# Kernel optimization log

Measured on AMD Instinct MI355X. Metric: run time of the kernel, lower is better.

The kernel has to match this reference:

```python
import jax, jax.numpy as jnp
import numpy as np

NUM_HEADS = 4
FEAT_DIM = 128
EMBED_DIM = 128
B, K, C, H, W = 2, 8, 128, 128, 128


def _cross_attn(Qf, Kf, Vf, qw, qb, kw, kb, aqw, aqb, akw, akb):
    """Faithful port of PixelCrossAttentionRefiner._cross_attn.
    Qf: [B, Cq, H, W]; Kf: [B, K, Ck, H, W]; Vf: [B, K, C, H, W].
    Uses only the (head-averaged) softmax weights of MultiheadAttention,
    L2-renormalizes them, then takes a weighted sum of RAW values.
    """
    b, _, h, w = Qf.shape
    k_cand = Kf.shape[1]
    bn = b * h * w
    # Query: per-pixel feature vector -> q1 projection -> attn in-proj (query part)
    Query = jnp.transpose(Qf, (0, 2, 3, 1)).reshape(bn, -1)            # [BN, Cq]
    q = Query @ qw.T + qb                                               # [BN, E]
    # Key: NOTE torch does .permute(0,1,3,4,2).reshape(B*N, K, -1) which is a
    # flat row-major reinterpretation of the (B,K,H,W,Ck) buffer; jnp reshape
    # after transpose has identical semantics, so this is bit-faithful.
    Key = jnp.transpose(Kf, (0, 1, 3, 4, 2)).reshape(bn, k_cand, -1)    # [BN, K, Ck]
    kk = Key @ kw.T + kb                                                # [BN, K, E]
    # nn.MultiheadAttention internal in-projections (value path is dead code)
    qa = q @ aqw.T + aqb                                                # [BN, E]
    ka = kk @ akw.T + akb                                               # [BN, K, E]
    e = qa.shape[-1]
    dh = e // NUM_HEADS
    qh = qa.reshape(bn, NUM_HEADS, dh)
    kh = ka.reshape(bn, k_cand, NUM_HEADS, dh)
    scale = 1.0 / np.sqrt(dh).astype(np.float32)
    scores = jnp.einsum('mhd,mkhd->mhk', qh, kh) * scale                # [BN, H, K]
    attw = jax.nn.softmax(scores, axis=-1).mean(axis=1)                 # avg heads -> [BN, K]
    # F.normalize(p=2, dim=-1, eps=1e-12)
    attw = attw / jnp.maximum(jnp.linalg.norm(attw, axis=-1, keepdims=True), 1e-12)
    Value = jnp.transpose(Vf, (0, 1, 3, 4, 2)).reshape(bn, k_cand, -1)  # [BN, K, C]
    out = jnp.einsum('mk,mkc->mc', attw, Value)                         # [BN, C]
    return jnp.transpose(out.reshape(b, h, w, -1), (0, 3, 1, 2))        # [B, C, H, W]


def _forward(HF_star, HF_cands, Z_cands,
             q1_w, q1_b, k1_w, k1_b, a1_qw, a1_qb, a1_kw, a1_kb,
             q2_w, q2_b, k2_w, k2_b, a2_qw, a2_qb, a2_kw, a2_kb):
    b, c, h, w = HF_star.shape
    k_cand = HF_cands.shape[1]
    i = jnp.linspace(0.0, 1.0, h, dtype=HF_star.dtype)
    j = jnp.linspace(0.0, 1.0, w, dtype=HF_star.dtype)
    ig, jg = jnp.meshgrid(i, j, indexing='ij')
    ig = jnp.broadcast_to(ig[None, None], (b, 1, h, w))
    jg = jnp.broadcast_to(jg[None, None], (b, 1, h, w))
    Q1 = jnp.concatenate([HF_star, ig, jg], axis=1)                     # [B, C+2, H, W]
    ik = jnp.broadcast_to(ig[:, None], (b, k_cand, 1, h, w))
    jk = jnp.broadcast_to(jg[:, None], (b, k_cand, 1, h, w))
    K1 = jnp.concatenate([HF_cands, ik, jk], axis=2)                    # [B, K, C+2, H, W]
    z_star = _cross_attn(Q1, K1, Z_cands, q1_w, q1_b, k1_w, k1_b,
                         a1_qw, a1_qb, a1_kw, a1_kb)                    # [B, C, H, W]
    z_exp = jnp.broadcast_to(z_star[:, None], (b, k_cand, c, h, w))
    Q2 = jnp.concatenate([HF_star, z_star, ig, jg], axis=1)             # [B, 2C+2, H, W]
    K2 = jnp.concatenate([HF_cands, z_exp, ik, jk], axis=2)             # [B, K, 2C+2, H, W]
    z_hat = _cross_attn(Q2, K2, Z_cands, q2_w, q2_b, k2_w, k2_b,
                        a2_qw, a2_qb, a2_kw, a2_kb)
    return z_star, z_hat


def setup_inputs() -> dict:
    key = jax.random.key(0)
    ks = jax.random.split(key, 16)
    E = EMBED_DIM
    d1 = FEAT_DIM + 2
    d2 = 2 * FEAT_DIM + 2

    def lin(k, fan_out, fan_in):
        bound = 1.0 / np.sqrt(fan_in)
        kw, kb = jax.random.split(k)
        return (jax.random.uniform(kw, (fan_out, fan_in), jnp.float32, -bound, bound),
                jax.random.uniform(kb, (fan_out,), jnp.float32, -bound, bound))

    q1_w, q1_b = lin(ks[0], E, d1)
    k1_w, k1_b = lin(ks[1], E, d1)
    q2_w, q2_b = lin(ks[2], E, d2)
    k2_w, k2_b = lin(ks[3], E, d2)
    a1_qw, a1_qb = lin(ks[4], E, E)
    a1_kw, a1_kb = lin(ks[5], E, E)
    a2_qw, a2_qb = lin(ks[6], E, E)
    a2_kw, a2_kb = lin(ks[7], E, E)
    return {
        'HF_star': jax.random.normal(ks[8], (B, C, H, W), jnp.float32),
        'HF_cands': jax.random.normal(ks[9], (B, K, C, H, W), jnp.float32),
        'Z_cands': jax.random.normal(ks[10], (B, K, C, H, W), jnp.float32),
        'q1_w': q1_w, 'q1_b': q1_b, 'k1_w': k1_w, 'k1_b': k1_b,
        'a1_qw': a1_qw, 'a1_qb': a1_qb, 'a1_kw': a1_kw, 'a1_kb': a1_kb,
        'q2_w': q2_w, 'q2_b': q2_b, 'k2_w': k2_w, 'k2_b': k2_b,
        'a2_qw': a2_qw, 'a2_qb': a2_qb, 'a2_kw': a2_kw, 'a2_kb': a2_kb,
    }


def reference(HF_star, HF_cands, Z_cands,
              q1_w, q1_b, k1_w, k1_b, a1_qw, a1_qb, a1_kw, a1_kb,
              q2_w, q2_b, k2_w, k2_b, a2_qw, a2_qb, a2_kw, a2_kb):
    return _forward(HF_star, HF_cands, Z_cands,
                    q1_w, q1_b, k1_w, k1_b, a1_qw, a1_qb, a1_kw, a1_kb,
                    q2_w, q2_b, k2_w, k2_b, a2_qw, a2_qb, a2_kw, a2_kb)
```

## Files before the change

### kernel.cpp

```cpp
#include <hip/hip_runtime.h>
#include <math.h>

constexpr int Bc = 2, Kc = 8, HWc = 16384;
constexpr float SCALE  = 0.17677669529663687f;
constexpr float INV127 = 1.0f / 127.0f;

using short8 = __attribute__((ext_vector_type(8))) short;
using f32x4  = __attribute__((ext_vector_type(4))) float;

constexpr int OWQ1 = 0;
constexpr int OBQ1 = OWQ1 + 130 * 128;
constexpr int OWK1 = OBQ1 + 128;
constexpr int OBK1 = OWK1 + 130 * 128;
constexpr int OWQ2 = OBK1 + 128;
constexpr int OBQ2 = OWQ2 + 258 * 128;
constexpr int OWK2 = OBQ2 + 128;
constexpr int OBK2 = OWK2 + 258 * 128;
constexpr int OPACK = OBK2 + 128;
constexpr int PQ1 = 0;
constexpr int PQ2 = PQ1 + 32 * 512;
constexpr int PY1 = PQ2 + 64 * 512;
constexpr int PY2 = PY1 + 32 * 512;

__device__ __forceinline__ unsigned bfpack(float a, float b) {
    unsigned ua = __float_as_uint(a); ua = (ua + 0x7FFFu + ((ua >> 16) & 1u)) >> 16;
    unsigned ub = __float_as_uint(b); ub = (ub + 0x7FFFu + ((ub >> 16) & 1u)) >> 16;
    return ua | (ub << 16);
}
__device__ __forceinline__ short bf1(float a) {
    unsigned ua = __float_as_uint(a); ua = (ua + 0x7FFFu + ((ua >> 16) & 1u)) >> 16;
    return (short)ua;
}
__device__ __forceinline__ float bflo(unsigned u) { return __uint_as_float(u << 16); }
__device__ __forceinline__ float bfhi(unsigned u) { return __uint_as_float(u & 0xFFFF0000u); }
__device__ __forceinline__ float bf2f(short s) {
    return __uint_as_float(((unsigned)(unsigned short)s) << 16);
}

__global__ __launch_bounds__(128) void prep_kernel(
    const float* __restrict__ q1w, const float* __restrict__ q1b,
    const float* __restrict__ k1w, const float* __restrict__ k1b,
    const float* __restrict__ a1qw, const float* __restrict__ a1qb,
    const float* __restrict__ a1kw, const float* __restrict__ a1kb,
    const float* __restrict__ q2w, const float* __restrict__ q2b,
    const float* __restrict__ k2w, const float* __restrict__ k2b,
    const float* __restrict__ a2qw, const float* __restrict__ a2qb,
    const float* __restrict__ a2kw, const float* __restrict__ a2kb,
    float* __restrict__ ws)
{
    const int job = blockIdx.x / 260;
    const int d   = blockIdx.x % 260;
    const float *aw, *ab, *w, *wb;
    float *owt, *ob;
    int D;
    if (job == 0)      { aw=a1qw; ab=a1qb; w=q1w; wb=q1b; owt=ws+OWQ1; ob=ws+OBQ1; D=130; }
    else if (job == 1) { aw=a1kw; ab=a1kb; w=k1w; wb=k1b; owt=ws+OWK1; ob=ws+OBK1; D=130; }
    else if (job == 2) { aw=a2qw; ab=a2qb; w=q2w; wb=q2b; owt=ws+OWQ2; ob=ws+OBQ2; D=258; }
    else               { aw=a2kw; ab=a2kb; w=k2w; wb=k2b; owt=ws+OWK2; ob=ws+OBK2; D=258; }
    const int e = threadIdx.x;
    if (d < D) {
        float acc = 0.f;
        for (int f = 0; f < 128; ++f) acc += aw[e * 128 + f] * w[f * D + d];
        owt[d * 128 + e] = acc;
    } else if (d == D) {
        float acc = ab[e];
        for (int f = 0; f < 128; ++f) acc += aw[e * 128 + f] * wb[f];
        ob[e] = acc;
    }
}

__global__ __launch_bounds__(64) void pack_kernel(float* __restrict__ ws)
{
    short* pk = (short*)(ws + OPACK);
    const int l = threadIdx.x, bid = blockIdx.x;
    const float* w;
    short* dst;
    short v[8];
    if (bid < 32) {
        const int et = bid >> 2, kt = bid & 3;
        w = ws + OWQ1;
        dst = pk + PQ1 + ((size_t)(et * 4 + kt) * 64 + l) * 8;
        #pragma unroll
        for (int idx = 0; idx < 8; ++idx)
            v[idx] = bf1(w[(kt * 32 + (l >> 4) * 8 + idx) * 128 + et * 16 + (l & 15)]);
    } else if (bid < 96) {
        const int b2 = bid - 32, et = b2 >> 3, kt = b2 & 7;
        w = ws + OWQ2;
        dst = pk + PQ2 + ((size_t)(et * 8 + kt) * 64 + l) * 8;
        #pragma unroll
        for (int idx = 0; idx < 8; ++idx)
            v[idx] = bf1(w[(kt * 32 + (l >> 4) * 8 + idx) * 128 + et * 16 + (l & 15)]);
    } else if (bid < 128) {
        const int b2 = bid - 96, ct = b2 >> 2, h = b2 & 3;
        w = ws + OWK1;
        dst = pk + PY1 + ((size_t)(ct * 4 + h) * 64 + l) * 8;
        #pragma unroll
        for (int idx = 0; idx < 8; ++idx)
            v[idx] = bf1(w[(ct * 16 + (l & 15)) * 128 + h * 32 + (l >> 4) * 8 + idx]);
    } else {
        const int b2 = bid - 128, ct = b2 >> 2, h = b2 & 3;
        w = ws + OWK2;
        dst = pk + PY2 + ((size_t)(ct * 4 + h) * 64 + l) * 8;
        #pragma unroll
        for (int idx = 0; idx < 8; ++idx)
            v[idx] = bf1(w[(ct * 16 + (l & 15)) * 128 + h * 32 + (l >> 4) * 8 + idx]);
    }
    uint4 u;
    u.x = (unsigned)(unsigned short)v[0] | ((unsigned)(unsigned short)v[1] << 16);
    u.y = (unsigned)(unsigned short)v[2] | ((unsigned)(unsigned short)v[3] << 16);
    u.z = (unsigned)(unsigned short)v[4] | ((unsigned)(unsigned short)v[5] << 16);
    u.w = (unsigned)(unsigned short)v[6] | ((unsigned)(unsigned short)v[7] << 16);
    *(uint4*)dst = u;
}

template <int STAGE>
__global__ __launch_bounds__(256) void stage_kernel(
    const float* __restrict__ HFs,
    const float* __restrict__ HFc,
    const float* __restrict__ Zc,
    const float* __restrict__ ws,
    const float* __restrict__ zst,
    float* __restrict__ out)
{
    constexpr int CQ  = (STAGE == 1) ? 128 : 256;
    constexpr int CK  = CQ;
    constexpr int NP  = CK / 128;
    constexpr int NKT = CQ / 32;

    const float* qwt = ws + ((STAGE == 1) ? OWQ1 : OWQ2);
    const float* qb_ = ws + ((STAGE == 1) ? OBQ1 : OBQ2);
    const float* kwt = ws + ((STAGE == 1) ? OWK1 : OWK2);
    const float* kb_ = ws + ((STAGE == 1) ? OBK1 : OBK2);
    const short* pk  = (const short*)(ws + OPACK);
    const short* aQ  = pk + ((STAGE == 1) ? PQ1 : PQ2);
    const short* aY  = pk + ((STAGE == 1) ? PY1 : PY2);

    __shared__ __align__(16) char smem[27136];
    short* sXF = (short*)smem;
    uint2* sYQ = (uint2*)smem;
    float* sRed = (float*)smem;
    short* sQF = (short*)(smem + 17408);
    float* sYX = (float*)(smem + 21504);
    float* sHW = sYX + 192;
    float* sSc = sHW + 576;
    float* sAW = sSc + 512;

    const int t   = threadIdx.x;
    const int l   = t & 63;
    const int wv  = t >> 6;
    const int bid = blockIdx.x;
    const int b   = bid >> 10;
    const int rem = bid & 1023;
    const int ks  = rem >> 7;
    const int hp  = rem & 127;
    const int r0  = ks * 2048 + hp * 16;

    const float ik = (float)hp * INV127;
    const float iq = (float)(r0 >> 7) * INV127;
    const int   w0 = r0 & 127;

    {
        const int qg = t & 3, c = t >> 2;
        #pragma unroll
        for (int r = 0; r < CQ / 64; ++r) {
            const int cc = c + r * 64;
            const float* src = (STAGE == 1 || cc < 128)
                ? HFs + ((size_t)(b * 128 + cc)) * HWc + r0 + qg * 4
                : zst + ((size_t)(b * 128 + (cc - 128))) * HWc + r0 + qg * 4;
            const float4 x = *(const float4*)src;
            const int kt = cc >> 5, g = (cc & 31) >> 3, idx = cc & 7;
            short* dstb = &sXF[kt * 512 + idx + 16 * g * 8];
            dstb[(qg * 4 + 0) * 8] = bf1(x.x);
            dstb[(qg * 4 + 1) * 8] = bf1(x.y);
            dstb[(qg * 4 + 2) * 8] = bf1(x.z);
            dstb[(qg * 4 + 3) * 8] = bf1(x.w);
        }
    }
    __syncthreads();

    {
        const float jqv = (float)(w0 + (l & 15)) * INV127;
        f32x4 acc0, acc1;
        #pragma unroll
        for (int r = 0; r < 4; ++r) {
            const int e0 = (wv * 2 + 0) * 16 + (l >> 4) * 4 + r;
            const int e1 = (wv * 2 + 1) * 16 + (l >> 4) * 4 + r;
            acc0[r] = qb_[e0] + iq * qwt[(size_t)CQ * 128 + e0]
                             + jqv * qwt[(size_t)(CQ + 1) * 128 + e0];
            acc1[r] = qb_[e1] + iq * qwt[(size_t)CQ * 128 + e1]
                             + jqv * qwt[(size_t)(CQ + 1) * 128 + e1];
        }
        #pragma unroll
        for (int kt = 0; kt < NKT; ++kt) {
            const short8 bfr = *(const short8*)&sXF[kt * 512 + l * 8];
            const short8 a0 = *(const short8*)&aQ[(((wv * 2 + 0) * NKT + kt) * 64 + l) * 8];
            const short8 a1 = *(const short8*)&aQ[(((wv * 2 + 1) * NKT + kt) * 64 + l) * 8];
            acc0 = __builtin_amdgcn_mfma_f32_16x16x32_bf16(a0, bfr, acc0, 0, 0, 0);
            acc1 = __builtin_amdgcn_mfma_f32_16x16x32_bf16(a1, bfr, acc1, 0, 0, 0);
        }
        #pragma unroll
        for (int m = 0; m < 2; ++m) {
            const f32x4 a = m ? acc1 : acc0;
            const int e0 = (wv * 2 + m) * 16 + (l >> 4) * 4;
            const int kt = e0 >> 5, g = (e0 & 31) >> 3, idx0 = e0 & 7;
            uint2 u; u.x = bfpack(a[0], a[1]); u.y = bfpack(a[2], a[3]);
            *(uint2*)&sQF[kt * 512 + ((l & 15) + 16 * g) * 8 + idx0] = u;
        }
    }
    __syncthreads();

    if (t < 192) {
        const int q = t & 15, h = (t >> 4) & 3, which = t >> 6;
        const float* wrow = (which == 0) ? kwt + (size_t)CK * 128
                          : (which == 1) ? kwt + (size_t)(CK + 1) * 128
                                         : kb_;
        float acc = 0.f;
        #pragma unroll
        for (int e32 = 0; e32 < 32; ++e32) {
            const int e2 = h * 32 + e32;
            const int g = (e2 & 31) >> 3, idx = e2 & 7;
            acc += wrow[e2] * bf2f(sQF[h * 512 + (q + 16 * g) * 8 + idx]);
        }
        sYX[(which * 4 + h) * 16 + q] = acc;
    }

    short8 bq0 = *(const short8*)&sQF[0 * 512 + l * 8];
    short8 bq1 = *(const short8*)&sQF[1 * 512 + l * 8];
    short8 bq2 = *(const short8*)&sQF[2 * 512 + l * 8];
    short8 bq3 = *(const short8*)&sQF[3 * 512 + l * 8];

    const int pg = t & 31;
    const int cs = t >> 5;
    const int q  = pg >> 1;
    float acc[4][4];
    #pragma unroll
    for (int h = 0; h < 4; ++h)
        #pragma unroll
        for (int j = 0; j < 4; ++j) acc[h][j] = 0.f;
    const f32x4 zf = {0.f, 0.f, 0.f, 0.f};

    #pragma unroll
    for (int p = 0; p < NP; ++p) {
        #pragma unroll
        for (int m = 0; m < 2; ++m) {
            const int ctl = wv * 2 + m;
            const int ct  = p * 8 + ctl;
            f32x4 d0, d1, d2, d3;
            {
                const short8 a0 = *(const short8*)&aY[(((ct * 4) + 0) * 64 + l) * 8];
                const short8 a1 = *(const short8*)&aY[(((ct * 4) + 1) * 64 + l) * 8];
                const short8 a2 = *(const short8*)&aY[(((ct * 4) + 2) * 64 + l) * 8];
                const short8 a3 = *(const short8*)&aY[(((ct * 4) + 3) * 64 + l) * 8];
                d0 = __builtin_amdgcn_mfma_f32_16x16x32_bf16(a0, bq0, zf, 0, 0, 0);
                d1 = __builtin_amdgcn_mfma_f32_16x16x32_bf16(a1, bq1, zf, 0, 0, 0);
                d2 = __builtin_amdgcn_mfma_f32_16x16x32_bf16(a2, bq2, zf, 0, 0, 0);
                d3 = __builtin_amdgcn_mfma_f32_16x16x32_bf16(a3, bq3, zf, 0, 0, 0);
            }
            #pragma unroll
            for (int r = 0; r < 4; ++r) {
                const int cl = ctl * 16 + (l >> 4) * 4 + r;
                uint2 u;
                u.x = bfpack(d0[r], d1[r]);
                u.y = bfpack(d2[r], d3[r]);
                sYQ[cl * 17 + (l & 15)] = u;
            }
        }
        __syncthreads();

        {
            const int cbase = p * 128 + cs * 16;
            const float* xp = (STAGE == 1 || cbase < 128)
                ? HFc + (((size_t)(b * Kc + ks)) * 128 + cbase) * HWc + hp * 128 + pg * 4
                : zst + ((size_t)(b * 128 + (cbase - 128))) * HWc + hp * 128 + pg * 4;
            const uint2* yqp = &sYQ[(cs * 16) * 17 + q];
            #pragma unroll 8
            for (int cc = 0; cc < 16; ++cc) {
                const float4 x = *(const float4*)(xp + (size_t)cc * HWc);
                const uint2 u = yqp[cc * 17];
                const float y0 = bflo(u.x), y1 = bfhi(u.x);
                const float y2 = bflo(u.y), y3 = bfhi(u.y);
                acc[0][0] += y0 * x.x; acc[0][1] += y0 * x.y;
                acc[0][2] += y0 * x.z; acc[0][3] += y0 * x.w;
                acc[1][0] += y1 * x.x; acc[1][1] += y1 * x.y;
                acc[1][2] += y1 * x.z; acc[1][3] += y1 * x.w;
                acc[2][0] += y2 * x.x; acc[2][1] += y2 * x.y;
                acc[2][2] += y2 * x.z; acc[2][3] += y2 * x.w;
                acc[3][0] += y3 * x.x; acc[3][1] += y3 * x.y;
                acc[3][2] += y3 * x.z; acc[3][3] += y3 * x.w;
            }
        }
        __syncthreads();
    }

    #pragma unroll
    for (int h = 0; h < 4; ++h)
        #pragma unroll
        for (int j = 0; j < 4; ++j)
            acc[h][j] += __shfl_xor(acc[h][j], 32, 64);
    if (l < 32) {
        #pragma unroll
        for (int h = 0; h < 4; ++h)
            #pragma unroll
            for (int j = 0; j < 4; ++j)
                sRed[wv * 512 + pg * 16 + h * 4 + j] = acc[h][j];
    }
    __syncthreads();

    if (t < 128) {
        const int pos = t, pgg = pos >> 2, j = pos & 3, qq = pos >> 3;
        const float jk = (float)pos * INV127;
        #pragma unroll
        for (int h = 0; h < 4; ++h) {
            const float v = sRed[0 * 512 + pgg * 16 + h * 4 + j]
                          + sRed[1 * 512 + pgg * 16 + h * 4 + j]
                          + sRed[2 * 512 + pgg * 16 + h * 4 + j]
                          + sRed[3 * 512 + pgg * 16 + h * 4 + j];
            const float s = v + ik * sYX[(0 * 4 + h) * 16 + qq]
                              + jk * sYX[(1 * 4 + h) * 16 + qq]
                              +      sYX[(2 * 4 + h) * 16 + qq];
            sSc[h * 128 + pos] = s * SCALE;
        }
    }
    __syncthreads();

    if (t < 64) {
        const int qq = t & 15, h = t >> 4;
        float sc[8], m = -INFINITY;
        #pragma unroll
        for (int j = 0; j < 8; ++j) {
            sc[j] = sSc[h * 128 + qq * 8 + j];
            m = fmaxf(m, sc[j]);
        }
        float sum = 0.f;
        #pragma unroll
        for (int j = 0; j < 8; ++j) { sc[j] = __expf(sc[j] - m); sum += sc[j]; }
        const float inv = 0.25f / sum;
        #pragma unroll
        for (int j = 0; j < 8; ++j) sHW[(h * 16 + qq) * 9 + j] = sc[j] * inv;
    }
    __syncthreads();
    if (t < 16) {
        float at[8];
        float n2 = 0.f;
        #pragma unroll
        for (int j = 0; j < 8; ++j) {
            at[j] = sHW[(0 * 16 + t) * 9 + j] + sHW[(1 * 16 + t) * 9 + j]
                  + sHW[(2 * 16 + t) * 9 + j] + sHW[(3 * 16 + t) * 9 + j];
            n2 += at[j] * at[j];
        }
        const float nrm = fmaxf(sqrtf(n2), 1e-12f);
        #pragma unroll
        for (int j = 0; j < 8; ++j) sAW[t * 8 + j] = at[j] / nrm;
    }
    __syncthreads();

    {
        const int idx = t & 15, cg = t >> 4;
        const int c8  = cg * 8;
        const float4 a0 = *(const float4*)&sAW[idx * 8];
        const float4 a1 = *(const float4*)&sAW[idx * 8 + 4];
        const float* zb = Zc + (((size_t)(b * Kc + ks)) * 128 + c8) * HWc + hp * 128 + idx * 8;
        float* ob = out + ((size_t)(b * 128 + c8)) * HWc + r0 + idx;
        #pragma unroll
        for (int i = 0; i < 8; ++i) {
            const float4 z0 = *(const float4*)(zb + (size_t)i * HWc);
            const float4 z1 = *(const float4*)(zb + (size_t)i * HWc + 4);
            ob[(size_t)i * HWc] =
                a0.x * z0.x + a0.y * z0.y + a0.z * z0.z + a0.w * z0.w +
                a1.x * z1.x + a1.y * z1.y + a1.z * z1.z + a1.w * z1.w;
        }
    }
}

extern "C" void kernel_launch(void* const* d_in, const int* in_sizes, int n_in,
                              void* d_out, int out_size, void* d_ws, size_t ws_size,
                              hipStream_t stream)
{
    const float* HFs = (const float*)d_in[0];
    const float* HFc = (const float*)d_in[1];
    const float* Zc  = (const float*)d_in[2];
    float* ws    = (float*)d_ws;
    float* zstar = (float*)d_out;
    float* zhat  = zstar + (size_t)Bc * 128 * HWc;

    prep_kernel<<<1040, 128, 0, stream>>>(
        (const float*)d_in[3],  (const float*)d_in[4],
        (const float*)d_in[5],  (const float*)d_in[6],
        (const float*)d_in[7],  (const float*)d_in[8],
        (const float*)d_in[9],  (const float*)d_in[10],
        (const float*)d_in[11], (const float*)d_in[12],
        (const float*)d_in[13], (const float*)d_in[14],
        (const float*)d_in[15], (const float*)d_in[16],
        (const float*)d_in[17], (const float*)d_in[18],
        ws);

    pack_kernel<<<192, 64, 0, stream>>>(ws);

    stage_kernel<1><<<2048, 256, 0, stream>>>(HFs, HFc, Zc, ws, zstar, zstar);
    stage_kernel<2><<<2048, 256, 0, stream>>>(HFs, HFc, Zc, ws, zstar, zhat);
}
```

Measured before the change: 154.7 us.

## Process two candidate slices per block to reuse weight fragments and zstar loads

Each block now handles two adjacent candidate indices (ks0, ks0+1), which halves the grid to 1024 blocks. The query-projection and key-projection MFMA fragments are loaded once and applied to both slices. In stage 2 the zstar channel half of the key input is loaded once and shared by both accumulators. The cost is roughly double the register and shared-memory footprint per block (46 KB of LDS), which may lower occupancy and leave fewer blocks to fill the GPU.

```diff
diff --git a/kernel.cpp b/kernel.cpp
--- a/kernel.cpp
+++ b/kernel.cpp
@@ -35,6 +35,14 @@
 __device__ __forceinline__ float bfhi(unsigned u) { return __uint_as_float(u & 0xFFFF0000u); }
 __device__ __forceinline__ float bf2f(short s) {
     return __uint_as_float(((unsigned)(unsigned short)s) << 16);
+}
+
+__device__ __forceinline__ void fma16(float (&a)[4][4], uint2 u, float4 x) {
+    const float y0 = bflo(u.x), y1 = bfhi(u.x), y2 = bflo(u.y), y3 = bfhi(u.y);
+    a[0][0] += y0 * x.x; a[0][1] += y0 * x.y; a[0][2] += y0 * x.z; a[0][3] += y0 * x.w;
+    a[1][0] += y1 * x.x; a[1][1] += y1 * x.y; a[1][2] += y1 * x.z; a[1][3] += y1 * x.w;
+    a[2][0] += y2 * x.x; a[2][1] += y2 * x.y; a[2][2] += y2 * x.z; a[2][3] += y2 * x.w;
+    a[3][0] += y3 * x.x; a[3][1] += y3 * x.y; a[3][2] += y3 * x.z; a[3][3] += y3 * x.w;
 }
 
 __global__ __launch_bounds__(128) void prep_kernel(
@@ -135,108 +143,135 @@
     const short* aQ  = pk + ((STAGE == 1) ? PQ1 : PQ2);
     const short* aY  = pk + ((STAGE == 1) ? PY1 : PY2);
 
-    __shared__ __align__(16) char smem[27136];
-    short* sXF = (short*)smem;
-    uint2* sYQ = (uint2*)smem;
+    __shared__ __align__(16) char smem[46080];
+    short* sXF0 = (short*)smem;
+    short* sXF1 = sXF0 + CQ * 16;
+    short* sQF0 = sXF0 + 2 * CQ * 16;
+    short* sQF1 = sQF0 + 2048;
+    uint2* sYQ0 = (uint2*)smem;
+    uint2* sYQ1 = sYQ0 + 128 * 17;
     float* sRed = (float*)smem;
-    short* sQF = (short*)(smem + 17408);
-    float* sYX = (float*)(smem + 21504);
-    float* sHW = sYX + 192;
-    float* sSc = sHW + 576;
-    float* sAW = sSc + 512;
+    float* sYX  = (float*)(smem + 34816);
+    float* sHW  = sYX + 384;
+    float* sSc  = sHW + 1152;
+    float* sAW  = sSc + 1024;
 
     const int t   = threadIdx.x;
     const int l   = t & 63;
     const int wv  = t >> 6;
     const int bid = blockIdx.x;
-    const int b   = bid >> 10;
-    const int rem = bid & 1023;
-    const int ks  = rem >> 7;
+    const int b   = bid >> 9;
+    const int rem = bid & 511;
+    const int kp  = rem >> 7;
     const int hp  = rem & 127;
-    const int r0  = ks * 2048 + hp * 16;
-
-    const float ik = (float)hp * INV127;
-    const float iq = (float)(r0 >> 7) * INV127;
-    const int   w0 = r0 & 127;
+    const int ks0 = kp * 2;
+    const int r00 = ks0 * 2048 + hp * 16;
+    const int r01 = r00 + 2048;
+
+    const float ik  = (float)hp * INV127;
+    const float iq0 = (float)(r00 >> 7) * INV127;
+    const float iq1 = (float)(r01 >> 7) * INV127;
+    const int   w0  = (hp & 7) * 16;
 
     {
         const int qg = t & 3, c = t >> 2;
         #pragma unroll
         for (int r = 0; r < CQ / 64; ++r) {
             const int cc = c + r * 64;
-            const float* src = (STAGE == 1 || cc < 128)
-                ? HFs + ((size_t)(b * 128 + cc)) * HWc + r0 + qg * 4
-                : zst + ((size_t)(b * 128 + (cc - 128))) * HWc + r0 + qg * 4;
-            const float4 x = *(const float4*)src;
             const int kt = cc >> 5, g = (cc & 31) >> 3, idx = cc & 7;
-            short* dstb = &sXF[kt * 512 + idx + 16 * g * 8];
-            dstb[(qg * 4 + 0) * 8] = bf1(x.x);
-            dstb[(qg * 4 + 1) * 8] = bf1(x.y);
-            dstb[(qg * 4 + 2) * 8] = bf1(x.z);
-            dstb[(qg * 4 + 3) * 8] = bf1(x.w);
+            #pragma unroll
+            for (int kk = 0; kk < 2; ++kk) {
+                const int r0 = kk ? r01 : r00;
+                const float* src = (STAGE == 1 || cc < 128)
+                    ? HFs + ((size_t)(b * 128 + cc)) * HWc + r0 + qg * 4
+                    : zst + ((size_t)(b * 128 + cc - 128)) * HWc + r0 + qg * 4;
+                const float4 x = *(const float4*)src;
+                short* dstb = (kk ? sXF1 : sXF0) + kt * 512 + idx + 16 * g * 8;
+                dstb[(qg * 4 + 0) * 8] = bf1(x.x);
+                dstb[(qg * 4 + 1) * 8] = bf1(x.y);
+                dstb[(qg * 4 + 2) * 8] = bf1(x.z);
+                dstb[(qg * 4 + 3) * 8] = bf1(x.w);
+            }
         }
     }
     __syncthreads();
 
     {
         const float jqv = (float)(w0 + (l & 15)) * INV127;
-        f32x4 acc0, acc1;
+        f32x4 a00, a01, a10, a11;
         #pragma unroll
         for (int r = 0; r < 4; ++r) {
             const int e0 = (wv * 2 + 0) * 16 + (l >> 4) * 4 + r;
             const int e1 = (wv * 2 + 1) * 16 + (l >> 4) * 4 + r;
-            acc0[r] = qb_[e0] + iq * qwt[(size_t)CQ * 128 + e0]
-                             + jqv * qwt[(size_t)(CQ + 1) * 128 + e0];
-            acc1[r] = qb_[e1] + iq * qwt[(size_t)CQ * 128 + e1]
-                             + jqv * qwt[(size_t)(CQ + 1) * 128 + e1];
+            const float wi0 = qwt[(size_t)CQ * 128 + e0];
+            const float wj0 = qwt[(size_t)(CQ + 1) * 128 + e0];
+            const float wi1 = qwt[(size_t)CQ * 128 + e1];
+            const float wj1 = qwt[(size_t)(CQ + 1) * 128 + e1];
+            a00[r] = qb_[e0] + iq0 * wi0 + jqv * wj0;
+            a01[r] = qb_[e1] + iq0 * wi1 + jqv * wj1;
+            a10[r] = qb_[e0] + iq1 * wi0 + jqv * wj0;
+            a11[r] = qb_[e1] + iq1 * wi1 + jqv * wj1;
         }
         #pragma unroll
         for (int kt = 0; kt < NKT; ++kt) {
-            const short8 bfr = *(const short8*)&sXF[kt * 512 + l * 8];
-            const short8 a0 = *(const short8*)&aQ[(((wv * 2 + 0) * NKT + kt) * 64 + l) * 8];
-            const short8 a1 = *(const short8*)&aQ[(((wv * 2 + 1) * NKT + kt) * 64 + l) * 8];
-            acc0 = __builtin_amdgcn_mfma_f32_16x16x32_bf16(a0, bfr, acc0, 0, 0, 0);
-            acc1 = __builtin_amdgcn_mfma_f32_16x16x32_bf16(a1, bfr, acc1, 0, 0, 0);
+            const short8 b0 = *(const short8*)&sXF0[kt * 512 + l * 8];
+            const short8 b1 = *(const short8*)&sXF1[kt * 512 + l * 8];
+            const short8 f0 = *(const short8*)&aQ[(((wv * 2 + 0) * NKT + kt) * 64 + l) * 8];
+            const short8 f1 = *(const short8*)&aQ[(((wv * 2 + 1) * NKT + kt) * 64 + l) * 8];
+            a00 = __builtin_amdgcn_mfma_f32_16x16x32_bf16(f0, b0, a00, 0, 0, 0);
+            a01 = __builtin_amdgcn_mfma_f32_16x16x32_bf16(f1, b0, a01, 0, 0, 0);
+            a10 = __builtin_amdgcn_mfma_f32_16x16x32_bf16(f0, b1, a10, 0, 0, 0);
+            a11 = __builtin_amdgcn_mfma_f32_16x16x32_bf16(f1, b1, a11, 0, 0, 0);
         }
         #pragma unroll
         for (int m = 0; m < 2; ++m) {
-            const f32x4 a = m ? acc1 : acc0;
             const int e0 = (wv * 2 + m) * 16 + (l >> 4) * 4;
             const int kt = e0 >> 5, g = (e0 & 31) >> 3, idx0 = e0 & 7;
-            uint2 u; u.x = bfpack(a[0], a[1]); u.y = bfpack(a[2], a[3]);
-            *(uint2*)&sQF[kt * 512 + ((l & 15) + 16 * g) * 8 + idx0] = u;
+            const f32x4 va = m ? a01 : a00;
+            const f32x4 vb = m ? a11 : a10;
+            uint2 u0; u0.x = bfpack(va[0], va[1]); u0.y = bfpack(va[2], va[3]);
+            uint2 u1; u1.x = bfpack(vb[0], vb[1]); u1.y = bfpack(vb[2], vb[3]);
+            *(uint2*)&sQF0[kt * 512 + ((l & 15) + 16 * g) * 8 + idx0] = u0;
+            *(uint2*)&sQF1[kt * 512 + ((l & 15) + 16 * g) * 8 + idx0] = u1;
         }
     }
     __syncthreads();
 
     if (t < 192) {
-        const int q = t & 15, h = (t >> 4) & 3, which = t >> 6;
+        const int qq = t & 15, h = (t >> 4) & 3, which = t >> 6;
         const float* wrow = (which == 0) ? kwt + (size_t)CK * 128
                           : (which == 1) ? kwt + (size_t)(CK + 1) * 128
                                          : kb_;
-        float acc = 0.f;
+        float acc0 = 0.f, acc1 = 0.f;
         #pragma unroll
         for (int e32 = 0; e32 < 32; ++e32) {
             const int e2 = h * 32 + e32;
             const int g = (e2 & 31) >> 3, idx = e2 & 7;
-            acc += wrow[e2] * bf2f(sQF[h * 512 + (q + 16 * g) * 8 + idx]);
-        }
-        sYX[(which * 4 + h) * 16 + q] = acc;
-    }
-
-    short8 bq0 = *(const short8*)&sQF[0 * 512 + l * 8];
-    short8 bq1 = *(const short8*)&sQF[1 * 512 + l * 8];
-    short8 bq2 = *(const short8*)&sQF[2 * 512 + l * 8];
-    short8 bq3 = *(const short8*)&sQF[3 * 512 + l * 8];
+            const float wr = wrow[e2];
+            acc0 += wr * bf2f(sQF0[h * 512 + (qq + 16 * g) * 8 + idx]);
+            acc1 += wr * bf2f(sQF1[h * 512 + (qq + 16 * g) * 8 + idx]);
+        }
+        sYX[0 * 192 + (which * 4 + h) * 16 + qq] = acc0;
+        sYX[1 * 192 + (which * 4 + h) * 16 + qq] = acc1;
+    }
+    const short8 bqa0 = *(const short8*)&sQF0[0 * 512 + l * 8];
+    const short8 bqa1 = *(const short8*)&sQF0[1 * 512 + l * 8];
+    const short8 bqa2 = *(const short8*)&sQF0[2 * 512 + l * 8];
+    const short8 bqa3 = *(const short8*)&sQF0[3 * 512 + l * 8];
+    const short8 bqb0 = *(const short8*)&sQF1[0 * 512 + l * 8];
+    const short8 bqb1 = *(const short8*)&sQF1[1 * 512 + l * 8];
+    const short8 bqb2 = *(const short8*)&sQF1[2 * 512 + l * 8];
+    const short8 bqb3 = *(const short8*)&sQF1[3 * 512 + l * 8];
+    __syncthreads();
 
     const int pg = t & 31;
     const int cs = t >> 5;
     const int q  = pg >> 1;
-    float acc[4][4];
+    float acc0[4][4], acc1[4][4];
     #pragma unroll
     for (int h = 0; h < 4; ++h)
         #pragma unroll
-        for (int j = 0; j < 4; ++j) acc[h][j] = 0.f;
+        for (int j = 0; j < 4; ++j) { acc0[h][j] = 0.f; acc1[h][j] = 0.f; }
     const f32x4 zf = {0.f, 0.f, 0.f, 0.f};
 
     #pragma unroll
@@ -245,48 +280,52 @@
         for (int m = 0; m < 2; ++m) {
             const int ctl = wv * 2 + m;
             const int ct  = p * 8 + ctl;
-            f32x4 d0, d1, d2, d3;
-            {
-                const short8 a0 = *(const short8*)&aY[(((ct * 4) + 0) * 64 + l) * 8];
-                const short8 a1 = *(const short8*)&aY[(((ct * 4) + 1) * 64 + l) * 8];
-                const short8 a2 = *(const short8*)&aY[(((ct * 4) + 2) * 64 + l) * 8];
-                const short8 a3 = *(const short8*)&aY[(((ct * 4) + 3) * 64 + l) * 8];
-                d0 = __builtin_amdgcn_mfma_f32_16x16x32_bf16(a0, bq0, zf, 0, 0, 0);
-                d1 = __builtin_amdgcn_mfma_f32_16x16x32_bf16(a1, bq1, zf, 0, 0, 0);
-                d2 = __builtin_amdgcn_mfma_f32_16x16x32_bf16(a2, bq2, zf, 0, 0, 0);
-                d3 = __builtin_amdgcn_mfma_f32_16x16x32_bf16(a3, bq3, zf, 0, 0, 0);
-            }
+            const short8 y0 = *(const short8*)&aY[(((ct * 4) + 0) * 64 + l) * 8];
+            const short8 y1 = *(const short8*)&aY[(((ct * 4) + 1) * 64 + l) * 8];
+            const short8 y2 = *(const short8*)&aY[(((ct * 4) + 2) * 64 + l) * 8];
+            const short8 y3 = *(const short8*)&aY[(((ct * 4) + 3) * 64 + l) * 8];
+            f32x4 d0 = __builtin_amdgcn_mfma_f32_16x16x32_bf16(y0, bqa0, zf, 0, 0, 0);
+            f32x4 d1 = __builtin_amdgcn_mfma_f32_16x16x32_bf16(y1, bqa1, zf, 0, 0, 0);
+            f32x4 d2 = __builtin_amdgcn_mfma_f32_16x16x32_bf16(y2, bqa2, zf, 0, 0, 0);
+            f32x4 d3 = __builtin_amdgcn_mfma_f32_16x16x32_bf16(y3, bqa3, zf, 0, 0, 0);
+            f32x4 e0 = __builtin_amdgcn_mfma_f32_16x16x32_bf16(y0, bqb0, zf, 0, 0, 0);
+            f32x4 e1 = __builtin_amdgcn_mfma_f32_16x16x32_bf16(y1, bqb1, zf, 0, 0, 0);
+            f32x4 e2 = __builtin_amdgcn_mfma_f32_16x16x32_bf16(y2, bqb2, zf, 0, 0, 0);
+            f32x4 e3 = __builtin_amdgcn_mfma_f32_16x16x32_bf16(y3, bqb3, zf, 0, 0, 0);
             #pragma unroll
             for (int r = 0; r < 4; ++r) {
                 const int cl = ctl * 16 + (l >> 4) * 4 + r;
-                uint2 u;
-                u.x = bfpack(d0[r], d1[r]);
-                u.y = bfpack(d2[r], d3[r]);
-                sYQ[cl * 17 + (l & 15)] = u;
+                uint2 u0; u0.x = bfpack(d0[r], d1[r]); u0.y = bfpack(d2[r], d3[r]);
+                uint2 u1; u1.x = bfpack(e0[r], e1[r]); u1.y = bfpack(e2[r], e3[r]);
+                sYQ0[cl * 17 + (l & 15)] = u0;
+                sYQ1[cl * 17 + (l & 15)] = u1;
             }
         }
         __syncthreads();
 
         {
-            const int cbase = p * 128 + cs * 16;
-            const float* xp = (STAGE == 1 || cbase < 128)
-                ? HFc + (((size_t)(b * Kc + ks)) * 128 + cbase) * HWc + hp * 128 + pg * 4
-                : zst + ((size_t)(b * 128 + (cbase - 128))) * HWc + hp * 128 + pg * 4;
-            const uint2* yqp = &sYQ[(cs * 16) * 17 + q];
-            #pragma unroll 8
-            for (int cc = 0; cc < 16; ++cc) {
-                const float4 x = *(const float4*)(xp + (size_t)cc * HWc);
-                const uint2 u = yqp[cc * 17];
-                const float y0 = bflo(u.x), y1 = bfhi(u.x);
-                const float y2 = bflo(u.y), y3 = bfhi(u.y);
-                acc[0][0] += y0 * x.x; acc[0][1] += y0 * x.y;
-                acc[0][2] += y0 * x.z; acc[0][3] += y0 * x.w;
-                acc[1][0] += y1 * x.x; acc[1][1] += y1 * x.y;
-                acc[1][2] += y1 * x.z; acc[1][3] += y1 * x.w;
-                acc[2][0] += y2 * x.x; acc[2][1] += y2 * x.y;
-                acc[2][2] += y2 * x.z; acc[2][3] += y2 * x.w;
-                acc[3][0] += y3 * x.x; acc[3][1] += y3 * x.y;
-                acc[3][2] += y3 * x.z; acc[3][3] += y3 * x.w;
+            const uint2* y0p = &sYQ0[(cs * 16) * 17 + q];
+            const uint2* y1p = &sYQ1[(cs * 16) * 17 + q];
+            if (STAGE == 1 || p == 0) {
+                const float* xp0 = HFc + (((size_t)(b * Kc + ks0)) * 128 + cs * 16) * HWc
+                                 + hp * 128 + pg * 4;
+                const float* xp1 = xp0 + (size_t)128 * HWc;
+                #pragma unroll 4
+                for (int cc = 0; cc < 16; ++cc) {
+                    const float4 x0 = *(const float4*)(xp0 + (size_t)cc * HWc);
+                    const float4 x1 = *(const float4*)(xp1 + (size_t)cc * HWc);
+                    fma16(acc0, y0p[cc * 17], x0);
+                    fma16(acc1, y1p[cc * 17], x1);
+                }
+            } else {
+                const float* xp = zst + ((size_t)(b * 128 + cs * 16)) * HWc
+                                + hp * 128 + pg * 4;
+                #pragma unroll 4
+                for (int cc = 0; cc < 16; ++cc) {
+                    const float4 x = *(const float4*)(xp + (size_t)cc * HWc);
+                    fma16(acc0, y0p[cc * 17], x);
+                    fma16(acc1, y1p[cc * 17], x);
+                }
             }
         }
         __syncthreads();
@@ -295,14 +334,18 @@
     #pragma unroll
     for (int h = 0; h < 4; ++h)
         #pragma unroll
-        for (int j = 0; j < 4; ++j)
-            acc[h][j] += __shfl_xor(acc[h][j], 32, 64);
+        for (int j = 0; j < 4; ++j) {
+            acc0[h][j] += __shfl_xor(acc0[h][j], 32, 64);
+            acc1[h][j] += __shfl_xor(acc1[h][j], 32, 64);
+        }
     if (l < 32) {
         #pragma unroll
         for (int h = 0; h < 4; ++h)
             #pragma unroll
-            for (int j = 0; j < 4; ++j)
-                sRed[wv * 512 + pg * 16 + h * 4 + j] = acc[h][j];
+            for (int j = 0; j < 4; ++j) {
+                sRed[wv * 1024 + pg * 32 + h * 4 + j]      = acc0[h][j];
+                sRed[wv * 1024 + pg * 32 + 16 + h * 4 + j] = acc1[h][j];
+            }
     }
     __syncthreads();
 
@@ -310,25 +353,29 @@
         const int pos = t, pgg = pos >> 2, j = pos & 3, qq = pos >> 3;
         const float jk = (float)pos * INV127;
         #pragma unroll
-        for (int h = 0; h < 4; ++h) {
-            const float v = sRed[0 * 512 + pgg * 16 + h * 4 + j]
-                          + sRed[1 * 512 + pgg * 16 + h * 4 + j]
-                          + sRed[2 * 512 + pgg * 16 + h * 4 + j]
-                          + sRed[3 * 512 + pgg * 16 + h * 4 + j];
-            const float s = v + ik * sYX[(0 * 4 + h) * 16 + qq]
-                              + jk * sYX[(1 * 4 + h) * 16 + qq]
-                              +      sYX[(2 * 4 + h) * 16 + qq];
-            sSc[h * 128 + pos] = s * SCALE;
-        }
-    }
-    __syncthreads();
-
-    if (t < 64) {
-        const int qq = t & 15, h = t >> 4;
+        for (int kk = 0; kk < 2; ++kk) {
+            #pragma unroll
+            for (int h = 0; h < 4; ++h) {
+                const float v = sRed[0 * 1024 + pgg * 32 + kk * 16 + h * 4 + j]
+                              + sRed[1 * 1024 + pgg * 32 + kk * 16 + h * 4 + j]
+                              + sRed[2 * 1024 + pgg * 32 + kk * 16 + h * 4 + j]
+                              + sRed[3 * 1024 + pgg * 32 + kk * 16 + h * 4 + j];
+                const float s = v + ik * sYX[kk * 192 + (0 * 4 + h) * 16 + qq]
+                                  + jk * sYX[kk * 192 + (1 * 4 + h) * 16 + qq]
+                                  +      sYX[kk * 192 + (2 * 4 + h) * 16 + qq];
+                sSc[kk * 512 + h * 128 + pos] = s * SCALE;
+            }
+        }
+    }
+    __syncthreads();
+
+    if (t < 128) {
+        const int kk = t >> 6, r = t & 63;
+        const int qq = r & 15, h = r >> 4;
         float sc[8], m = -INFINITY;
         #pragma unroll
         for (int j = 0; j < 8; ++j) {
-            sc[j] = sSc[h * 128 + qq * 8 + j];
+            sc[j] = sSc[kk * 512 + h * 128 + qq * 8 + j];
             m = fmaxf(m, sc[j]);
         }
         float sum = 0.f;
@@ -336,38 +383,47 @@
         for (int j = 0; j < 8; ++j) { sc[j] = __expf(sc[j] - m); sum += sc[j]; }
         const float inv = 0.25f / sum;
         #pragma unroll
-        for (int j = 0; j < 8; ++j) sHW[(h * 16 + qq) * 9 + j] = sc[j] * inv;
-    }
-    __syncthreads();
-    if (t < 16) {
+        for (int j = 0; j < 8; ++j) sHW[kk * 576 + (h * 16 + qq) * 9 + j] = sc[j] * inv;
+    }
+    __syncthreads();
+    if (t < 32) {
+        const int kk = t >> 4, qq = t & 15;
         float at[8];
         float n2 = 0.f;
         #pragma unroll
         for (int j = 0; j < 8; ++j) {
-            at[j] = sHW[(0 * 16 + t) * 9 + j] + sHW[(1 * 16 + t) * 9 + j]
-                  + sHW[(2 * 16 + t) * 9 + j] + sHW[(3 * 16 + t) * 9 + j];
+            at[j] = sHW[kk * 576 + (0 * 16 + qq) * 9 + j]
+                  + sHW[kk * 576 + (1 * 16 + qq) * 9 + j]
+                  + sHW[kk * 576 + (2 * 16 + qq) * 9 + j]
+                  + sHW[kk * 576 + (3 * 16 + qq) * 9 + j];
             n2 += at[j] * at[j];
         }
         const float nrm = fmaxf(sqrtf(n2), 1e-12f);
         #pragma unroll
-        for (int j = 0; j < 8; ++j) sAW[t * 8 + j] = at[j] / nrm;
+        for (int j = 0; j < 8; ++j) sAW[kk * 128 + qq * 8 + j] = at[j] / nrm;
     }
     __syncthreads();
 
     {
         const int idx = t & 15, cg = t >> 4;
         const int c8  = cg * 8;
-        const float4 a0 = *(const float4*)&sAW[idx * 8];
-        const float4 a1 = *(const float4*)&sAW[idx * 8 + 4];
-        const float* zb = Zc + (((size_t)(b * Kc + ks)) * 128 + c8) * HWc + hp * 128 + idx * 8;
-        float* ob = out + ((size_t)(b * 128 + c8)) * HWc + r0 + idx;
-        #pragma unroll
-        for (int i = 0; i < 8; ++i) {
-            const float4 z0 = *(const float4*)(zb + (size_t)i * HWc);
-            const float4 z1 = *(const float4*)(zb + (size_t)i * HWc + 4);
-            ob[(size_t)i * HWc] =
-                a0.x * z0.x + a0.y * z0.y + a0.z * z0.z + a0.w * z0.w +
-                a1.x * z1.x + a1.y * z1.y + a1.z * z1.z + a1.w * z1.w;
+        #pragma unroll
+        for (int kk = 0; kk < 2; ++kk) {
+            const int ks = ks0 + kk;
+            const int r0 = kk ? r01 : r00;
+            const float4 a0 = *(const float4*)&sAW[kk * 128 + idx * 8];
+            const float4 a1 = *(const float4*)&sAW[kk * 128 + idx * 8 + 4];
+            const float* zb = Zc + (((size_t)(b * Kc + ks)) * 128 + c8) * HWc
+                            + hp * 128 + idx * 8;
+            float* ob = out + ((size_t)(b * 128 + c8)) * HWc + r0 + idx;
+            #pragma unroll
+            for (int i = 0; i < 8; ++i) {
+                const float4 z0 = *(const float4*)(zb + (size_t)i * HWc);
+                const float4 z1 = *(const float4*)(zb + (size_t)i * HWc + 4);
+                ob[(size_t)i * HWc] =
+                    a0.x * z0.x + a0.y * z0.y + a0.z * z0.z + a0.w * z0.w +
+                    a1.x * z1.x + a1.y * z1.y + a1.z * z1.z + a1.w * z1.w;
+            }
         }
     }
 }
@@ -396,6 +452,6 @@
 
     pack_kernel<<<192, 64, 0, stream>>>(ws);
 
-    stage_kernel<1><<<2048, 256, 0, stream>>>(HFs, HFc, Zc, ws, zstar, zstar);
-    stage_kernel<2><<<2048, 256, 0, stream>>>(HFs, HFc, Zc, ws, zstar, zhat);
-}
+    stage_kernel<1><<<1024, 256, 0, stream>>>(HFs, HFc, Zc, ws, zstar, zstar);
+    stage_kernel<2><<<1024, 256, 0, stream>>>(HFs, HFc, Zc, ws, zstar, zhat);
+}
```

Measured after the change: 154.8 us. No clear change (+0.0%).
